# Performance work log

Hardware: AMD Instinct MI355X
Metric: run time of the kernel (lower is better)

Reference implementation:

```python
import jax, jax.numpy as jnp
import numpy as np

NUM_HEADS = 64          # also the positional-embedding size (quirk of the module)
DIM_IN, DIM_K, DIM_V = 512, 512, 64
BATCH, SEQ = 4, 1024


def setup_inputs() -> dict:
    key = jax.random.key(0)
    ks = jax.random.split(key, 7)
    s = 0.05  # weight init scale
    return {
        "x":  jax.random.normal(ks[0], (BATCH, SEQ, DIM_IN), jnp.float32),
        "Wq": jax.random.normal(ks[1], (DIM_IN, DIM_K), jnp.float32) * s,
        "bq": jax.random.normal(ks[2], (DIM_K,), jnp.float32) * s,
        "Wk": jax.random.normal(ks[3], (DIM_IN, DIM_K), jnp.float32) * s,
        "bk": jax.random.normal(ks[4], (DIM_K,), jnp.float32) * s,
        "Wv": jax.random.normal(ks[5], (DIM_IN, DIM_V), jnp.float32) * s,
        "bv": jax.random.normal(ks[6], (DIM_V,), jnp.float32) * s,
    }


def _position_embedding(n, position_size):
    # matches Position_Enbedding: cos block then sin block along feature dim
    half = position_size // 2
    pos_j = 1.0 / jnp.power(10000.0, 2.0 * jnp.arange(half, dtype=jnp.float32) / position_size)
    pos_ij = jnp.arange(n, dtype=jnp.float32)[:, None] * pos_j[None, :]   # [n, half]
    return jnp.concatenate([jnp.cos(pos_ij), jnp.sin(pos_ij)], axis=1)    # [n, position_size]


def reference(x, Wq, bq, Wk, bk, Wv, bv):
    B, n, _ = x.shape
    nh = NUM_HEADS
    dk = DIM_K // nh   # 8
    dv = DIM_V // nh   # 1
    # fused linear + ReLU, then split heads: [B, nh, n, d]
    q = jax.nn.relu(x @ Wq + bq).reshape(B, n, nh, dk).transpose(0, 2, 1, 3)
    k = jax.nn.relu(x @ Wk + bk).reshape(B, n, nh, dk).transpose(0, 2, 1, 3)
    v = jax.nn.relu(x @ Wv + bv).reshape(B, n, nh, dv).transpose(0, 2, 1, 3)
    scale = 1.0 / np.sqrt(dk).astype(np.float32)
    dist = jax.nn.softmax(jnp.einsum('bhqd,bhkd->bhqk', q, k) * scale, axis=-1)
    att = jnp.einsum('bhqk,bhkd->bhqd', dist, v)            # [B, nh, n, dv]
    att = att.transpose(0, 2, 1, 3).reshape(B, n, DIM_V)    # [B, n, dim_v]
    pe = _position_embedding(n, nh)                          # [n, nh] == [n, dim_v]
    return att + pe[None, :, :]
```

## Files before the change

kernel.cpp:

```cpp
#include <hip/hip_runtime.h>
#include <math.h>

#define BATCH 4
#define SEQ   1024
#define DIN   512
#define DKQ   512
#define DV    64
#define NH    64

typedef __attribute__((ext_vector_type(8))) short short8v;
typedef __attribute__((ext_vector_type(4))) float float4v;
typedef __attribute__((ext_vector_type(4))) unsigned int uint4v;

__device__ __forceinline__ void split_bf16(float f, unsigned short& hi, unsigned short& lo) {
    unsigned int u = __float_as_uint(f);
    hi = (unsigned short)(u >> 16);
    float l = f - __uint_as_float(u & 0xFFFF0000u);
    lo = (unsigned short)(__float_as_uint(l) >> 16);
}
__device__ __forceinline__ unsigned short f32_to_bf16_rne(float f) {
    unsigned int u = __float_as_uint(f);
    u += 0x7FFFu + ((u >> 16) & 1u);
    return (unsigned short)(u >> 16);
}
__device__ __forceinline__ float bf16_bits_to_f32(unsigned short s) {
    return __uint_as_float((unsigned int)s << 16);
}

__device__ __forceinline__ void gll16(const unsigned short* g, unsigned short* l) {
    __builtin_amdgcn_global_load_lds(
        (const __attribute__((address_space(1))) unsigned int*)(g),
        (__attribute__((address_space(3))) unsigned int*)(l),
        16, 0, 0);
}

__global__ __launch_bounds__(256)
void pack_x(const float* __restrict__ x,
            unsigned short* __restrict__ Xhi, unsigned short* __restrict__ Xlo,
            unsigned int* __restrict__ obuf)
{
    if (blockIdx.x == 0 && threadIdx.x < 8)
        obuf[threadIdx.x] = (threadIdx.x < 4) ? 0x3F803F80u : 0u;
    const int i = (blockIdx.x * 256 + threadIdx.x) * 8;
    float4 a0 = *(const float4*)&x[i];
    float4 a1 = *(const float4*)&x[i + 4];
    float av[8] = {a0.x, a0.y, a0.z, a0.w, a1.x, a1.y, a1.z, a1.w};
    short8v h, l;
    #pragma unroll
    for (int j = 0; j < 8; ++j) {
        unsigned short hh, ll; split_bf16(av[j], hh, ll);
        h[j] = (short)hh; l[j] = (short)ll;
    }
    *(short8v*)&Xhi[i] = h;
    *(short8v*)&Xlo[i] = l;
}

__global__ __launch_bounds__(256)
void transpose_w(const float* __restrict__ Wq, const float* __restrict__ Wk,
                 const float* __restrict__ Wv,
                 unsigned short* __restrict__ WhiQ, unsigned short* __restrict__ WloQ,
                 unsigned short* __restrict__ WhiK, unsigned short* __restrict__ WloK,
                 unsigned short* __restrict__ WhiV, unsigned short* __restrict__ WloV)
{
    const int z = blockIdx.z;
    const int N = (z == 2) ? DV : DKQ;
    if (z == 2 && blockIdx.x >= 2) return;
    const float* __restrict__ W = (z == 0) ? Wq : (z == 1) ? Wk : Wv;
    unsigned short* __restrict__ Whi = (z == 0) ? WhiQ : (z == 1) ? WhiK : WhiV;
    unsigned short* __restrict__ Wlo = (z == 0) ? WloQ : (z == 1) ? WloK : WloV;

    __shared__ float tile[32][33];
    const int n0 = blockIdx.x * 32, k0 = blockIdx.y * 32;
    const int tx = threadIdx.x, ty = threadIdx.y;
    #pragma unroll
    for (int i = 0; i < 32; i += 8)
        tile[ty + i][tx] = W[(size_t)(k0 + ty + i) * N + n0 + tx];
    __syncthreads();
    #pragma unroll
    for (int i = 0; i < 32; i += 8) {
        unsigned short h, l; split_bf16(tile[tx][ty + i], h, l);
        Whi[(size_t)(n0 + ty + i) * DIN + k0 + tx] = h;
        Wlo[(size_t)(n0 + ty + i) * DIN + k0 + tx] = l;
    }
}

__global__ __launch_bounds__(512)
void proj_kernel(const unsigned short* __restrict__ Xhi,
                 const unsigned short* __restrict__ Xlo,
                 const unsigned short* __restrict__ WhiQ, const unsigned short* __restrict__ WloQ,
                 const float* __restrict__ bq,
                 const unsigned short* __restrict__ WhiK, const unsigned short* __restrict__ WloK,
                 const float* __restrict__ bk,
                 const unsigned short* __restrict__ WhiV, const unsigned short* __restrict__ WloV,
                 const float* __restrict__ bv,
                 unsigned short* __restrict__ Qpk, unsigned short* __restrict__ Kpk,
                 unsigned int* __restrict__ Vsh, unsigned int* __restrict__ Vsl)
{
    const int z = blockIdx.z;
    if (z == 2 && blockIdx.x != 0) return;
    const unsigned short* __restrict__ Whi = (z == 0) ? WhiQ : (z == 1) ? WhiK : WhiV;
    const unsigned short* __restrict__ Wlo = (z == 0) ? WloQ : (z == 1) ? WloK : WloV;
    const float* __restrict__ bias = (z == 0) ? bq : (z == 1) ? bk : bv;

    __shared__ unsigned short LDS[2][16384];

    const int t = threadIdx.x;
    const int wave = t >> 6, lane = t & 63;
    const int cl = lane & 15, g2 = lane >> 4;
    const int bm  = blockIdx.y * 128;
    const int cbb = (z == 2) ? 0 : blockIdx.x * 128;
    const int wr = wave >> 2, wc = wave & 3;
    const int NF = (z == 2) ? 1 : 2;

    const unsigned short* sAh = Xhi + (size_t)(bm + wave * 16 + cl) * DIN + g2 * 8;
    const unsigned short* sAl = Xlo + (size_t)(bm + wave * 16 + cl) * DIN + g2 * 8;
    const bool bvalid = (z != 2) || (wave < 4);
    const size_t bro = (size_t)(cbb + wave * 16 + cl) * DIN + g2 * 8;
    const unsigned short* sBh = Whi + (bvalid ? bro : 0);
    const unsigned short* sBl = Wlo + (bvalid ? bro : 0);

    float4v acc[4][2];
    #pragma unroll
    for (int i = 0; i < 4; ++i)
        #pragma unroll
        for (int j = 0; j < 2; ++j)
            acc[i][j] = (float4v){0.f, 0.f, 0.f, 0.f};

    {
        unsigned short* L = &LDS[0][0];
        gll16(sAh, L + (wave) * 512);
        gll16(sAl, L + (wave + 8) * 512);
        if (bvalid) {
            gll16(sBh, L + (wave + 16) * 512);
            gll16(sBl, L + (wave + 24) * 512);
        }
    }
    __syncthreads();

    for (int ks = 0; ks < 16; ++ks) {
        const int cur = ks & 1;
        if (ks < 15) {
            const int kn = (ks + 1) * 32;
            unsigned short* L = &LDS[cur ^ 1][0];
            gll16(sAh + kn, L + (wave) * 512);
            gll16(sAl + kn, L + (wave + 8) * 512);
            if (bvalid) {
                gll16(sBh + kn, L + (wave + 16) * 512);
                gll16(sBl + kn, L + (wave + 24) * 512);
            }
        }
        const unsigned short* L = &LDS[cur][0];
        short8v af_h[4], af_l[4], bf_h[2], bf_l[2];
        #pragma unroll
        for (int mt = 0; mt < 4; ++mt) {
            af_h[mt] = *(const short8v*)(L + (wr * 4 + mt) * 512 + lane * 8);
            af_l[mt] = *(const short8v*)(L + (8 + wr * 4 + mt) * 512 + lane * 8);
        }
        #pragma unroll
        for (int nf = 0; nf < 2; ++nf) {
            if (nf < NF) {
                bf_h[nf] = *(const short8v*)(L + (16 + wc * NF + nf) * 512 + lane * 8);
                bf_l[nf] = *(const short8v*)(L + (24 + wc * NF + nf) * 512 + lane * 8);
            }
        }
        #pragma unroll
        for (int mt = 0; mt < 4; ++mt)
            #pragma unroll
            for (int nf = 0; nf < 2; ++nf) {
                if (nf >= NF) continue;
                acc[mt][nf] = __builtin_amdgcn_mfma_f32_16x16x32_bf16(af_h[mt], bf_h[nf], acc[mt][nf], 0, 0, 0);
                acc[mt][nf] = __builtin_amdgcn_mfma_f32_16x16x32_bf16(af_l[mt], bf_h[nf], acc[mt][nf], 0, 0, 0);
                acc[mt][nf] = __builtin_amdgcn_mfma_f32_16x16x32_bf16(af_h[mt], bf_l[nf], acc[mt][nf], 0, 0, 0);
            }
        __syncthreads();
    }

    const float cc = 0.35355339059327373f * 1.4426950408889634f;
    if (z == 2) {
        const int n = wc * 16 + cl;
        const float bn = bias[n];
        #pragma unroll
        for (int mt = 0; mt < 4; ++mt) {
            const int row0 = bm + wr * 64 + mt * 16 + g2 * 4;
            const int bb = row0 >> 10, s0 = row0 & 1023;
            const int idx0 = (s0 >> 5) * 16 + ((s0 >> 2) & 3) * 4 + ((s0 >> 4) & 1) * 2;
            float vv[4]; unsigned short hh[4], ll[4];
            #pragma unroll
            for (int r = 0; r < 4; ++r) {
                vv[r] = fmaxf(acc[mt][0][r] + bn, 0.0f);
                hh[r] = f32_to_bf16_rne(vv[r]);
                ll[r] = f32_to_bf16_rne(vv[r] - bf16_bits_to_f32(hh[r]));
            }
            const size_t base = (size_t)((bb << 6) + n) * 512 + idx0;
            Vsh[base]     = (unsigned int)hh[0] | ((unsigned int)hh[1] << 16);
            Vsh[base + 1] = (unsigned int)hh[2] | ((unsigned int)hh[3] << 16);
            Vsl[base]     = (unsigned int)ll[0] | ((unsigned int)ll[1] << 16);
            Vsl[base + 1] = (unsigned int)ll[2] | ((unsigned int)ll[3] << 16);
        }
    } else {
        unsigned short* __restrict__ dst = (z == 0) ? Qpk : Kpk;
        #pragma unroll
        for (int nf = 0; nf < 2; ++nf) {
            const int n = cbb + wc * 32 + nf * 16 + cl;
            const float bn = bias[n];
            const int h = n >> 3, d = n & 7;
            #pragma unroll
            for (int mt = 0; mt < 4; ++mt) {
                #pragma unroll
                for (int r = 0; r < 4; ++r) {
                    const int row = bm + wr * 64 + mt * 16 + g2 * 4 + r;
                    const int bb = row >> 10, s = row & 1023;
                    float val = fmaxf(acc[mt][nf][r] + bn, 0.0f);
                    if (z == 0) val *= cc;
                    const size_t base = ((size_t)((bb << 6) + h) * SEQ + s) * 16 + d;
                    unsigned short hi = f32_to_bf16_rne(val);
                    dst[base]     = hi;
                    dst[base + 8] = f32_to_bf16_rne(val - bf16_bits_to_f32(hi));
                }
            }
        }
    }
}

__global__ __launch_bounds__(256, 4)
void attn_kernel(const unsigned short* __restrict__ Qpk,
                 const unsigned short* __restrict__ Kpk,
                 const unsigned int* __restrict__ Vsh,
                 const unsigned int* __restrict__ Vsl,
                 const unsigned int* __restrict__ obuf,
                 float2* __restrict__ part)
{
    const int bh = blockIdx.x;
    const int yb = blockIdx.y;
    const int qchunk = yb >> 2;
    const int kq = yb & 3;
    const int t = threadIdx.x;
    const int wave = t >> 6, lane = t & 63;
    const int g = lane >> 4, cl = lane & 15;

    const unsigned short* __restrict__ qb = Qpk + (size_t)bh * SEQ * 16;
    const unsigned short* __restrict__ kb = Kpk + (size_t)bh * SEQ * 16;

    const int q0 = qchunk * 256 + wave * 64;

    short8v bq[4];
    #pragma unroll
    for (int qt = 0; qt < 4; ++qt) {
        if (g == 3) { short8v zz = {0,0,0,0,0,0,0,0}; bq[qt] = zz; }
        else bq[qt] = *(const short8v*)(qb + (size_t)(q0 + qt * 16 + cl) * 16 + ((g == 1) ? 8 : 0));
    }

    const int koff = (g >> 1) * 8;
    const unsigned short* kp = kb + kq * 4096 + cl * 16 + koff;

    const unsigned int* ap;
    int astr;
    {
        const size_t vb = (size_t)bh * 512 + kq * 128 + g * 4;
        if (cl == 0)      { ap = Vsh + vb; astr = 16; }
        else if (cl == 2) { ap = Vsl + vb; astr = 16; }
        else if (cl == 1) { ap = obuf;     astr = 0;  }
        else              { ap = obuf + 4; astr = 0;  }
    }

    const float4v c0 = {0.f, 0.f, 0.f, 0.f};
    float4v acc[4];
    #pragma unroll
    for (int qt = 0; qt < 4; ++qt) acc[qt] = c0;

    short8v k0c = *(const short8v*)kp;
    short8v k1c = *(const short8v*)(kp + 256);
    uint4v  auc = *(const uint4v*)ap;

    #pragma unroll
    for (int ss = 0; ss < 8; ++ss) {
        short8v k0n, k1n; uint4v aun;
        if (ss < 7) {
            k0n = *(const short8v*)(kp + 512);
            k1n = *(const short8v*)(kp + 768);
            aun = *(const uint4v*)(ap + astr);
        }
        kp += 512; ap += astr;
        const short8v af = __builtin_bit_cast(short8v, auc);
        #pragma unroll
        for (int qt = 0; qt < 4; ++qt) {
            float4v s0 = __builtin_amdgcn_mfma_f32_16x16x32_bf16(k0c, bq[qt], c0, 0, 0, 0);
            float4v s1 = __builtin_amdgcn_mfma_f32_16x16x32_bf16(k1c, bq[qt], c0, 0, 0, 0);
            float p00 = __builtin_amdgcn_exp2f(s0[0]);
            float p01 = __builtin_amdgcn_exp2f(s0[1]);
            float p02 = __builtin_amdgcn_exp2f(s0[2]);
            float p03 = __builtin_amdgcn_exp2f(s0[3]);
            float p10 = __builtin_amdgcn_exp2f(s1[0]);
            float p11 = __builtin_amdgcn_exp2f(s1[1]);
            float p12 = __builtin_amdgcn_exp2f(s1[2]);
            float p13 = __builtin_amdgcn_exp2f(s1[3]);
            unsigned int pk0 = __builtin_amdgcn_perm(__float_as_uint(p01), __float_as_uint(p00), 0x07060302u);
            unsigned int pk1 = __builtin_amdgcn_perm(__float_as_uint(p03), __float_as_uint(p02), 0x07060302u);
            unsigned int pk2 = __builtin_amdgcn_perm(__float_as_uint(p11), __float_as_uint(p10), 0x07060302u);
            unsigned int pk3 = __builtin_amdgcn_perm(__float_as_uint(p13), __float_as_uint(p12), 0x07060302u);
            uint4v pu = {pk0, pk1, pk2, pk3};
            acc[qt] = __builtin_amdgcn_mfma_f32_16x16x32_bf16(af, __builtin_bit_cast(short8v, pu), acc[qt], 0, 0, 0);
        }
        if (ss < 7) { k0c = k0n; k1c = k1n; auc = aun; }
    }

    if (g == 0) {
        #pragma unroll
        for (int qt = 0; qt < 4; ++qt) {
            const int row = q0 + qt * 16 + cl;
            float2 pr;
            pr.x = acc[qt][0] + acc[qt][2];
            pr.y = acc[qt][1];
            part[(size_t)(kq * 256 + bh) * SEQ + row] = pr;
        }
    }
}

__global__ __launch_bounds__(256)
void merge_kernel(const float2* __restrict__ part, float* __restrict__ out)
{
    const int tid = blockIdx.x * 256 + threadIdx.x;
    const int h = tid & 63;
    const int q = (tid >> 6) & 1023;
    const int b = tid >> 16;
    const int bh = (b << 6) + h;
    float num = 0.f, den = 0.f;
    #pragma unroll
    for (int kq = 0; kq < 4; ++kq) {
        float2 p = part[(size_t)(kq * 256 + bh) * SEQ + q];
        num += p.x; den += p.y;
    }
    const float fr = __builtin_amdgcn_exp2f((float)(h & 31) * -0.4152410118609203f);
    const float pe = (h < 32) ? cosf((float)q * fr) : sinf((float)q * fr);
    out[tid] = num / den + pe;
}

extern "C" void kernel_launch(void* const* d_in, const int* in_sizes, int n_in,
                              void* d_out, int out_size, void* d_ws, size_t ws_size,
                              hipStream_t stream)
{
    const float* x  = (const float*)d_in[0];
    const float* Wq = (const float*)d_in[1];
    const float* bq = (const float*)d_in[2];
    const float* Wk = (const float*)d_in[3];
    const float* bk = (const float*)d_in[4];
    const float* Wv = (const float*)d_in[5];
    const float* bv = (const float*)d_in[6];
    float* out = (float*)d_out;

    unsigned short* Qpk = (unsigned short*)d_ws;
    unsigned short* Kpk = Qpk + (size_t)BATCH * NH * SEQ * 16;
    unsigned int* Vsh = (unsigned int*)(Kpk + (size_t)BATCH * NH * SEQ * 16);
    unsigned int* Vsl = Vsh + (size_t)BATCH * NH * (SEQ / 2);
    unsigned int* obuf = Vsl + (size_t)BATCH * NH * (SEQ / 2);
    unsigned short* Xhi = (unsigned short*)(obuf + 64);
    unsigned short* Xlo = Xhi + (size_t)BATCH * SEQ * DIN;
    float2* part = (float2*)Xhi;
    unsigned short* WhiQ = Xlo + (size_t)BATCH * SEQ * DIN;
    unsigned short* WloQ = WhiQ + (size_t)DIN * DKQ;
    unsigned short* WhiK = WloQ + (size_t)DIN * DKQ;
    unsigned short* WloK = WhiK + (size_t)DIN * DKQ;
    unsigned short* WhiV = WloK + (size_t)DIN * DKQ;
    unsigned short* WloV = WhiV + (size_t)DIN * DV;

    pack_x<<<dim3((BATCH * SEQ * DIN) / (8 * 256)), 256, 0, stream>>>(x, Xhi, Xlo, obuf);
    transpose_w<<<dim3(16, 16, 3), dim3(32, 8), 0, stream>>>(
        Wq, Wk, Wv, WhiQ, WloQ, WhiK, WloK, WhiV, WloV);
    proj_kernel<<<dim3(4, 32, 3), 512, 0, stream>>>(
        Xhi, Xlo, WhiQ, WloQ, bq, WhiK, WloK, bk, WhiV, WloV, bv, Qpk, Kpk, Vsh, Vsl);
    attn_kernel<<<dim3(256, 16), 256, 0, stream>>>(Qpk, Kpk, Vsh, Vsl, obuf, part);
    merge_kernel<<<dim3((BATCH * SEQ * DV) / 256), 256, 0, stream>>>(part, out);
}
```

Baseline: 83.31 us.

## Merge prepack kernels and triple-buffer projection GEMM with explicit vmcnt waits

Folds the x bf16-split kernel and the weight transpose kernel into a single launch, using an extra grid z-slice for the x packing, which removes one kernel launch. The projection GEMM moves from double to triple-buffered LDS with a prefetch distance of two k-steps. It replaces __syncthreads with explicit s_waitcnt vmcnt counts plus raw s_barrier, so the global-to-LDS loads overlap more MFMA work. This uses more LDS per block, which can lower occupancy, and it relies on hand-counted outstanding loads being correct.

Measured after the change: 84.85 us. About the same (+1.9%).

```diff
diff --git a/kernel.cpp b/kernel.cpp
--- a/kernel.cpp
+++ b/kernel.cpp
@@ -34,35 +34,44 @@
         16, 0, 0);
 }
 
+__device__ __forceinline__ void waitv4() { asm volatile("s_waitcnt vmcnt(4)" ::: "memory"); }
+__device__ __forceinline__ void waitv2() { asm volatile("s_waitcnt vmcnt(2)" ::: "memory"); }
+__device__ __forceinline__ void waitv0() { asm volatile("s_waitcnt vmcnt(0)" ::: "memory"); }
+
 __global__ __launch_bounds__(256)
-void pack_x(const float* __restrict__ x,
-            unsigned short* __restrict__ Xhi, unsigned short* __restrict__ Xlo,
-            unsigned int* __restrict__ obuf)
-{
-    if (blockIdx.x == 0 && threadIdx.x < 8)
-        obuf[threadIdx.x] = (threadIdx.x < 4) ? 0x3F803F80u : 0u;
-    const int i = (blockIdx.x * 256 + threadIdx.x) * 8;
-    float4 a0 = *(const float4*)&x[i];
-    float4 a1 = *(const float4*)&x[i + 4];
-    float av[8] = {a0.x, a0.y, a0.z, a0.w, a1.x, a1.y, a1.z, a1.w};
-    short8v h, l;
-    #pragma unroll
-    for (int j = 0; j < 8; ++j) {
-        unsigned short hh, ll; split_bf16(av[j], hh, ll);
-        h[j] = (short)hh; l[j] = (short)ll;
-    }
-    *(short8v*)&Xhi[i] = h;
-    *(short8v*)&Xlo[i] = l;
-}
-
-__global__ __launch_bounds__(256)
-void transpose_w(const float* __restrict__ Wq, const float* __restrict__ Wk,
-                 const float* __restrict__ Wv,
-                 unsigned short* __restrict__ WhiQ, unsigned short* __restrict__ WloQ,
-                 unsigned short* __restrict__ WhiK, unsigned short* __restrict__ WloK,
-                 unsigned short* __restrict__ WhiV, unsigned short* __restrict__ WloV)
+void prepack(const float* __restrict__ x,
+             const float* __restrict__ Wq, const float* __restrict__ Wk,
+             const float* __restrict__ Wv,
+             unsigned short* __restrict__ WhiQ, unsigned short* __restrict__ WloQ,
+             unsigned short* __restrict__ WhiK, unsigned short* __restrict__ WloK,
+             unsigned short* __restrict__ WhiV, unsigned short* __restrict__ WloV,
+             unsigned short* __restrict__ Xhi, unsigned short* __restrict__ Xlo,
+             unsigned int* __restrict__ obuf)
 {
     const int z = blockIdx.z;
+    const int tx = threadIdx.x, ty = threadIdx.y;
+    if (z == 3) {
+        const int t = ty * 32 + tx;
+        const int bid = blockIdx.y * 16 + blockIdx.x;
+        if (bid == 0 && t < 8)
+            obuf[t] = (t < 4) ? 0x3F803F80u : 0u;
+        #pragma unroll
+        for (int j = 0; j < 4; ++j) {
+            const int i = ((bid * 4 + j) * 256 + t) * 8;
+            float4 a0 = *(const float4*)&x[i];
+            float4 a1 = *(const float4*)&x[i + 4];
+            float av[8] = {a0.x, a0.y, a0.z, a0.w, a1.x, a1.y, a1.z, a1.w};
+            short8v h, l;
+            #pragma unroll
+            for (int jj = 0; jj < 8; ++jj) {
+                unsigned short hh, ll; split_bf16(av[jj], hh, ll);
+                h[jj] = (short)hh; l[jj] = (short)ll;
+            }
+            *(short8v*)&Xhi[i] = h;
+            *(short8v*)&Xlo[i] = l;
+        }
+        return;
+    }
     const int N = (z == 2) ? DV : DKQ;
     if (z == 2 && blockIdx.x >= 2) return;
     const float* __restrict__ W = (z == 0) ? Wq : (z == 1) ? Wk : Wv;
@@ -71,7 +80,6 @@
 
     __shared__ float tile[32][33];
     const int n0 = blockIdx.x * 32, k0 = blockIdx.y * 32;
-    const int tx = threadIdx.x, ty = threadIdx.y;
     #pragma unroll
     for (int i = 0; i < 32; i += 8)
         tile[ty + i][tx] = W[(size_t)(k0 + ty + i) * N + n0 + tx];
@@ -102,7 +110,7 @@
     const unsigned short* __restrict__ Wlo = (z == 0) ? WloQ : (z == 1) ? WloK : WloV;
     const float* __restrict__ bias = (z == 0) ? bq : (z == 1) ? bk : bv;
 
-    __shared__ unsigned short LDS[2][16384];
+    __shared__ unsigned short LDS[3][16384];
 
     const int t = threadIdx.x;
     const int wave = t >> 6, lane = t & 63;
@@ -119,6 +127,17 @@
     const unsigned short* sBh = Whi + (bvalid ? bro : 0);
     const unsigned short* sBl = Wlo + (bvalid ? bro : 0);
 
+    auto stage = [&](int step, int bufIdx) {
+        unsigned short* L = &LDS[bufIdx][0];
+        const int kofs = step * 32;
+        gll16(sAh + kofs, L + (wave) * 512);
+        gll16(sAl + kofs, L + (wave + 8) * 512);
+        if (bvalid) {
+            gll16(sBh + kofs, L + (wave + 16) * 512);
+            gll16(sBl + kofs, L + (wave + 24) * 512);
+        }
+    };
+
     float4v acc[4][2];
     #pragma unroll
     for (int i = 0; i < 4; ++i)
@@ -126,30 +145,17 @@
         for (int j = 0; j < 2; ++j)
             acc[i][j] = (float4v){0.f, 0.f, 0.f, 0.f};
 
-    {
-        unsigned short* L = &LDS[0][0];
-        gll16(sAh, L + (wave) * 512);
-        gll16(sAl, L + (wave + 8) * 512);
-        if (bvalid) {
-            gll16(sBh, L + (wave + 16) * 512);
-            gll16(sBl, L + (wave + 24) * 512);
-        }
-    }
-    __syncthreads();
-
+    stage(0, 0);
+    stage(1, 1);
+    if (bvalid) waitv4(); else waitv2();
+    __builtin_amdgcn_s_barrier();
+    __builtin_amdgcn_sched_barrier(0);
+
+    #pragma unroll
     for (int ks = 0; ks < 16; ++ks) {
-        const int cur = ks & 1;
-        if (ks < 15) {
-            const int kn = (ks + 1) * 32;
-            unsigned short* L = &LDS[cur ^ 1][0];
-            gll16(sAh + kn, L + (wave) * 512);
-            gll16(sAl + kn, L + (wave + 8) * 512);
-            if (bvalid) {
-                gll16(sBh + kn, L + (wave + 16) * 512);
-                gll16(sBl + kn, L + (wave + 24) * 512);
-            }
-        }
-        const unsigned short* L = &LDS[cur][0];
+        if (ks + 2 < 16) stage(ks + 2, (ks + 2) % 3);
+
+        const unsigned short* L = &LDS[ks % 3][0];
         short8v af_h[4], af_l[4], bf_h[2], bf_l[2];
         #pragma unroll
         for (int mt = 0; mt < 4; ++mt) {
@@ -172,7 +178,11 @@
                 acc[mt][nf] = __builtin_amdgcn_mfma_f32_16x16x32_bf16(af_l[mt], bf_h[nf], acc[mt][nf], 0, 0, 0);
                 acc[mt][nf] = __builtin_amdgcn_mfma_f32_16x16x32_bf16(af_h[mt], bf_l[nf], acc[mt][nf], 0, 0, 0);
             }
-        __syncthreads();
+
+        if (ks < 14) { if (bvalid) waitv4(); else waitv2(); }
+        else waitv0();
+        __builtin_amdgcn_s_barrier();
+        __builtin_amdgcn_sched_barrier(0);
     }
 
     const float cc = 0.35355339059327373f * 1.4426950408889634f;
@@ -363,9 +373,8 @@
     unsigned short* WhiV = WloK + (size_t)DIN * DKQ;
     unsigned short* WloV = WhiV + (size_t)DIN * DV;
 
-    pack_x<<<dim3((BATCH * SEQ * DIN) / (8 * 256)), 256, 0, stream>>>(x, Xhi, Xlo, obuf);
-    transpose_w<<<dim3(16, 16, 3), dim3(32, 8), 0, stream>>>(
-        Wq, Wk, Wv, WhiQ, WloQ, WhiK, WloK, WhiV, WloV);
+    prepack<<<dim3(16, 16, 4), dim3(32, 8), 0, stream>>>(
+        x, Wq, Wk, Wv, WhiQ, WloQ, WhiK, WloK, WhiV, WloV, Xhi, Xlo, obuf);
     proj_kernel<<<dim3(4, 32, 3), 512, 0, stream>>>(
         Xhi, Xlo, WhiQ, WloQ, bq, WhiK, WloK, bk, WhiV, WloV, bv, Qpk, Kpk, Vsh, Vsl);
     attn_kernel<<<dim3(256, 16), 256, 0, stream>>>(Qpk, Kpk, Vsh, Vsl, obuf, part);
```
